# Performance work log

Measured on AMD Instinct MI355X. Metric: run time of the kernel, lower is better.

## Reference

```python
import jax, jax.numpy as jnp
import numpy as np

IN_F = 1024
OUT_F = 1024

def setup_inputs() -> dict:
    key = jax.random.key(0)
    ks = jax.random.split(key, 7)
    s = 1.0 / np.sqrt(IN_F)
    x = jax.random.normal(ks[0], (4, 2048, IN_F), dtype=jnp.float32)
    Wq = jax.random.uniform(ks[1], (OUT_F, IN_F), jnp.float32, -s, s)
    bq = jax.random.uniform(ks[2], (OUT_F,), jnp.float32, -s, s)
    Wk = jax.random.uniform(ks[3], (OUT_F, IN_F), jnp.float32, -s, s)
    bk = jax.random.uniform(ks[4], (OUT_F,), jnp.float32, -s, s)
    Wv = jax.random.uniform(ks[5], (OUT_F, IN_F), jnp.float32, -s, s)
    bv = jax.random.uniform(ks[6], (OUT_F,), jnp.float32, -s, s)
    return {"x": x, "Wq": Wq, "bq": bq, "Wk": Wk, "bk": bk, "Wv": Wv, "bv": bv}

def reference(x, Wq, bq, Wk, bk, Wv, bv):
    # Projector: ReLU(Linear(x))
    q = jax.nn.relu(jnp.einsum('bsd,od->bso', x, Wq) + bq)  # [B,S,O]
    k = jax.nn.relu(jnp.einsum('bsd,od->bso', x, Wk) + bk)
    v = jax.nn.relu(jnp.einsum('bsd,od->bso', x, Wv) + bv)
    logits = jnp.einsum('bio,bko->bik', q, k)  # unscaled QK^T, [B,S,S]
    scores = jax.nn.softmax(logits, axis=-1)
    out = jnp.einsum('bik,bko->bio', scores, v)
    return out
```

## Files before the change

kernel.cpp:

```cpp
#include <hip/hip_runtime.h>
#include <hip/hip_bf16.h>


#define SEQ 2048
#define DIM 1024
#define NB 4
#define MTOT (NB * SEQ)

typedef __attribute__((ext_vector_type(8))) short frag_ab;
typedef __attribute__((ext_vector_type(16))) float frag_c16;

__device__ __forceinline__ ushort f2bf(float f) {
    union { float f; unsigned u; } x; x.f = f;
    unsigned r = x.u + 0x7fffu + ((x.u >> 16) & 1u);
    return (ushort)(r >> 16);
}

typedef __attribute__((address_space(1))) const unsigned int guint;
typedef __attribute__((address_space(3))) unsigned int luint;

__device__ __forceinline__ void gld_lds16(const void* g, void* l) {
    __builtin_amdgcn_global_load_lds((guint*)g, (luint*)l, 16, 0, 0);
}

__device__ __forceinline__ void gemm_tiles(
    const ushort* __restrict__ A, size_t lda,
    const ushort* __restrict__ B, size_t ldb, int K,
    ushort* As, ushort* Bs, frag_c16 (&acc)[2][2])
{
    const int tid  = threadIdx.x;
    const int wave = tid >> 6;
    const int lane = tid & 63;
    const int l32  = lane & 31;
    const int half = lane >> 5;
    const int sr = wave * 16 + (lane >> 2);
    const int sc = lane & 3;
    const int wm = (wave & 1) * 64;
    const int wn = (wave >> 1) * 64;

    for (int k0 = 0; k0 < K; k0 += 32) {
        #pragma unroll
        for (int j = 0; j < 2; ++j) {
            int row = j * 64 + sr;
            int cg  = sc ^ ((row >> 1) & 3);
            ushort* la = As + (j * 64 + wave * 16) * 32;
            ushort* lb = Bs + (j * 64 + wave * 16) * 32;
            gld_lds16(A + (size_t)row * lda + k0 + cg * 8, la);
            gld_lds16(B + (size_t)row * ldb + k0 + cg * 8, lb);
        }
        __syncthreads();
        frag_ab af[2][2], bfr[2][2];
        #pragma unroll
        for (int mi = 0; mi < 2; ++mi) {
            int row = wm + mi * 32 + l32;
            int sw = (row >> 1) & 3;
            #pragma unroll
            for (int h = 0; h < 2; ++h) {
                int c = (h * 2 + half) ^ sw;
                af[mi][h] = *(const frag_ab*)&As[row * 32 + c * 8];
            }
        }
        #pragma unroll
        for (int ni = 0; ni < 2; ++ni) {
            int row = wn + ni * 32 + l32;
            int sw = (row >> 1) & 3;
            #pragma unroll
            for (int h = 0; h < 2; ++h) {
                int c = (h * 2 + half) ^ sw;
                bfr[ni][h] = *(const frag_ab*)&Bs[row * 32 + c * 8];
            }
        }
        #pragma unroll
        for (int h = 0; h < 2; ++h)
            #pragma unroll
            for (int mi = 0; mi < 2; ++mi)
                #pragma unroll
                for (int ni = 0; ni < 2; ++ni)
                    acc[mi][ni] = __builtin_amdgcn_mfma_f32_32x32x16_bf16(
                        af[mi][h], bfr[ni][h], acc[mi][ni], 0, 0, 0);
        __syncthreads();
    }
}


#define NX4 (MTOT * DIM / 4)
#define NW4 (DIM * DIM / 4)
__global__ __launch_bounds__(256) void cvt_kernel(
    const float* __restrict__ x,
    const float* __restrict__ Wq, const float* __restrict__ Wk,
    const float* __restrict__ Wv,
    ushort* __restrict__ xb, ushort* __restrict__ Wb)
{
    size_t i = (size_t)blockIdx.x * 256 + threadIdx.x;
    const float* src; ushort* dst; size_t idx;
    if (i < NX4) { src = x; dst = xb; idx = i; }
    else {
        size_t j = i - NX4;
        int w = (int)(j >> 18);
        idx = j & (NW4 - 1);
        src = w == 0 ? Wq : (w == 1 ? Wk : Wv);
        dst = Wb + (size_t)w * DIM * DIM;
    }
    float4 f = ((const float4*)src)[idx];
    ushort4 u; u.x = f2bf(f.x); u.y = f2bf(f.y); u.z = f2bf(f.z); u.w = f2bf(f.w);
    ((ushort4*)dst)[idx] = u;
}

__global__ __launch_bounds__(256) void qkv_kernel(
    const ushort* __restrict__ xb, const ushort* __restrict__ Wb,
    const float* __restrict__ bq, const float* __restrict__ bk,
    const float* __restrict__ bv,
    ushort* __restrict__ q, ushort* __restrict__ kk, ushort* __restrict__ vt)
{
    const float* bias;
    if (blockIdx.z == 0)      bias = bq;
    else if (blockIdx.z == 1) bias = bk;
    else                      bias = bv;
    const ushort* W = Wb + (size_t)blockIdx.z * DIM * DIM;

    __shared__ ushort As[128 * 32];
    __shared__ ushort Bs[128 * 32];

    const int tid  = threadIdx.x;
    const int wave = tid >> 6;
    const int lane = tid & 63;
    const int l32  = lane & 31;
    const int half = lane >> 5;
    const int m0 = blockIdx.x * 128;
    const int n0 = blockIdx.y * 128;
    const int wm = (wave & 1) * 64;
    const int wn = (wave >> 1) * 64;

    frag_c16 acc[2][2] = {};
    gemm_tiles(xb + (size_t)m0 * DIM, DIM, W + (size_t)n0 * DIM, DIM, DIM,
               As, Bs, acc);

    if (blockIdx.z == 2) {
        const int bz = m0 >> 11;
        const int sb = (m0 & (SEQ - 1)) + wm;
        #pragma unroll
        for (int ni = 0; ni < 2; ++ni) {
            int col = n0 + wn + ni * 32 + l32;
            float bb = bias[col];
            ushort* vrow = vt + ((size_t)(bz * DIM + col)) * SEQ;
            #pragma unroll
            for (int mi = 0; mi < 2; ++mi)
                #pragma unroll
                for (int g = 0; g < 4; ++g) {
                    int s0 = sb + mi * 32 + 8 * g + 4 * half;
                    ushort4 u;
                    #pragma unroll
                    for (int j = 0; j < 4; ++j) {
                        float val = acc[mi][ni][4 * g + j] + bb;
                        val = val > 0.0f ? val : 0.0f;
                        ((ushort*)&u)[j] = f2bf(val);
                    }
                    *(ushort4*)&vrow[s0] = u;
                }
        }
    } else {
        ushort* out = blockIdx.z == 0 ? q : kk;
        #pragma unroll
        for (int ni = 0; ni < 2; ++ni) {
            int col = n0 + wn + ni * 32 + l32;
            float bb = bias[col];
            #pragma unroll
            for (int mi = 0; mi < 2; ++mi)
                #pragma unroll
                for (int r = 0; r < 16; ++r) {
                    int row = m0 + wm + mi * 32 + (r & 3) + 8 * (r >> 2) + 4 * half;
                    float val = acc[mi][ni][r] + bb;
                    val = val > 0.0f ? val : 0.0f;
                    out[(size_t)row * DIM + col] = f2bf(val);
                }
        }
    }
}

__global__ __launch_bounds__(256) void qk_kernel(
    const ushort* __restrict__ q, const ushort* __restrict__ kk,
    float* __restrict__ logits)
{
    __shared__ ushort As[128 * 32];
    __shared__ ushort Bs[128 * 32];

    const int tid  = threadIdx.x;
    const int wave = tid >> 6;
    const int lane = tid & 63;
    const int l32  = lane & 31;
    const int half = lane >> 5;
    const int bz = blockIdx.z;
    const int m0 = blockIdx.x * 128;
    const int n0 = blockIdx.y * 128;
    const int wm = (wave & 1) * 64;
    const int wn = (wave >> 1) * 64;
    const size_t base = (size_t)bz * SEQ;

    frag_c16 acc[2][2] = {};
    gemm_tiles(q + (base + m0) * DIM, DIM, kk + (base + n0) * DIM, DIM, DIM,
               As, Bs, acc);

    #pragma unroll
    for (int mi = 0; mi < 2; ++mi)
        #pragma unroll
        for (int r = 0; r < 16; ++r) {
            int row = m0 + wm + mi * 32 + (r & 3) + 8 * (r >> 2) + 4 * half;
            #pragma unroll
            for (int ni = 0; ni < 2; ++ni) {
                int col = n0 + wn + ni * 32 + l32;
                logits[(base + row) * SEQ + col] = acc[mi][ni][r];
            }
        }
}

__global__ __launch_bounds__(256) void softmax_kernel(float* __restrict__ logits)
{
    const int row  = blockIdx.x * 4 + (threadIdx.x >> 6);
    const int lane = threadIdx.x & 63;
    float* p = logits + (size_t)row * SEQ;

    float4 x[8];
    #pragma unroll
    for (int i = 0; i < 8; ++i) x[i] = ((const float4*)p)[lane + 64 * i];

    float m = -3.4e38f;
    #pragma unroll
    for (int i = 0; i < 8; ++i)
        m = fmaxf(m, fmaxf(fmaxf(x[i].x, x[i].y), fmaxf(x[i].z, x[i].w)));
    #pragma unroll
    for (int off = 32; off; off >>= 1) m = fmaxf(m, __shfl_xor(m, off, 64));

    float s = 0.0f;
    #pragma unroll
    for (int i = 0; i < 8; ++i) {
        x[i].x = __expf(x[i].x - m); x[i].y = __expf(x[i].y - m);
        x[i].z = __expf(x[i].z - m); x[i].w = __expf(x[i].w - m);
        s += (x[i].x + x[i].y) + (x[i].z + x[i].w);
    }
    #pragma unroll
    for (int off = 32; off; off >>= 1) s += __shfl_xor(s, off, 64);
    float inv = 1.0f / s;

    ushort* o = (ushort*)p;
    #pragma unroll
    for (int i = 0; i < 8; ++i) {
        ushort4 u;
        u.x = f2bf(x[i].x * inv); u.y = f2bf(x[i].y * inv);
        u.z = f2bf(x[i].z * inv); u.w = f2bf(x[i].w * inv);
        ((ushort4*)o)[lane + 64 * i] = u;
    }
}

__global__ __launch_bounds__(256) void pv_kernel(
    const ushort* __restrict__ probs, const ushort* __restrict__ vt,
    float* __restrict__ out)
{
    __shared__ ushort As[128 * 32];
    __shared__ ushort Bs[128 * 32];

    const int tid  = threadIdx.x;
    const int wave = tid >> 6;
    const int lane = tid & 63;
    const int l32  = lane & 31;
    const int half = lane >> 5;
    const int bz = blockIdx.z;
    const int m0 = blockIdx.x * 128;
    const int n0 = blockIdx.y * 128;
    const int wm = (wave & 1) * 64;
    const int wn = (wave >> 1) * 64;

    frag_c16 acc[2][2] = {};
    gemm_tiles(probs + ((size_t)(bz * SEQ + m0)) * 4096, 4096,
               vt + ((size_t)(bz * DIM + n0)) * SEQ, SEQ, SEQ,
               As, Bs, acc);

    #pragma unroll
    for (int mi = 0; mi < 2; ++mi)
        #pragma unroll
        for (int r = 0; r < 16; ++r) {
            int row = m0 + wm + mi * 32 + (r & 3) + 8 * (r >> 2) + 4 * half;
            #pragma unroll
            for (int ni = 0; ni < 2; ++ni) {
                int col = n0 + wn + ni * 32 + l32;
                out[((size_t)(bz * SEQ + row)) * DIM + col] = acc[mi][ni][r];
            }
        }
}

extern "C" void kernel_launch(void* const* d_in, const int* in_sizes, int n_in,
                              void* d_out, int out_size, void* d_ws, size_t ws_size,
                              hipStream_t stream)
{
    const float* x  = (const float*)d_in[0];
    const float* Wq = (const float*)d_in[1];
    const float* bq = (const float*)d_in[2];
    const float* Wk = (const float*)d_in[3];
    const float* bk = (const float*)d_in[4];
    const float* Wv = (const float*)d_in[5];
    const float* bv = (const float*)d_in[6];
    float* out = (float*)d_out;

    char* ws = (char*)d_ws;
    ushort* q      = (ushort*)(ws);
    ushort* kk     = (ushort*)(ws + ((size_t)16 << 20));
    ushort* vt     = (ushort*)(ws + ((size_t)48 << 20));
    float*  logits = (float*) (ws + ((size_t)64 << 20));
    ushort* xb     = (ushort*)(ws + ((size_t)64 << 20));
    ushort* Wb     = (ushort*)(ws + ((size_t)80 << 20));

    cvt_kernel<<<dim3((NX4 + 3 * NW4) / 256), 256, 0, stream>>>(
        x, Wq, Wk, Wv, xb, Wb);

    qkv_kernel<<<dim3(MTOT / 128, DIM / 128, 3), 256, 0, stream>>>(
        xb, Wb, bq, bk, bv, q, kk, vt);
    qk_kernel<<<dim3(SEQ / 128, SEQ / 128, NB), 256, 0, stream>>>(q, kk, logits);
    softmax_kernel<<<NB * SEQ / 4, 256, 0, stream>>>(logits);
    pv_kernel<<<dim3(SEQ / 128, DIM / 128, NB), 256, 0, stream>>>(
        (const ushort*)logits, vt, out);
}
```

Measured before the change: 280.4 us.

## Double-buffer LDS tiles in shared GEMM loop with async prefetch

The shared GEMM tile loop now uses two LDS buffers. It issues the global-to-LDS loads for the next K tile before computing on the current one, waits with an explicit vmcnt and uses raw s_barrier instead of two __syncthreads per iteration. This is meant to hide global load latency behind MFMA work in the projection, QK and PV kernels. It doubles LDS use per block, which may lower occupancy, and the final iteration issues a redundant reload of the last tile.

Result: slower. 292.5 us (+4.3%).

```diff
diff --git a/kernel.cpp b/kernel.cpp
--- a/kernel.cpp
+++ b/kernel.cpp
@@ -22,6 +22,15 @@
 __device__ __forceinline__ void gld_lds16(const void* g, void* l) {
     __builtin_amdgcn_global_load_lds((guint*)g, (luint*)l, 16, 0, 0);
 }
+
+__device__ __forceinline__ void bar() {
+    asm volatile("" ::: "memory");
+    __builtin_amdgcn_s_barrier();
+    asm volatile("" ::: "memory");
+}
+#define VMCNT(n) asm volatile("s_waitcnt vmcnt(" #n ")" ::: "memory")
+
+#define TB (128 * 32)
 
 __device__ __forceinline__ void gemm_tiles(
     const ushort* __restrict__ A, size_t lda,
@@ -37,18 +46,31 @@
     const int sc = lane & 3;
     const int wm = (wave & 1) * 64;
     const int wn = (wave >> 1) * 64;
-
-    for (int k0 = 0; k0 < K; k0 += 32) {
-        #pragma unroll
-        for (int j = 0; j < 2; ++j) {
-            int row = j * 64 + sr;
-            int cg  = sc ^ ((row >> 1) & 3);
-            ushort* la = As + (j * 64 + wave * 16) * 32;
-            ushort* lb = Bs + (j * 64 + wave * 16) * 32;
-            gld_lds16(A + (size_t)row * lda + k0 + cg * 8, la);
-            gld_lds16(B + (size_t)row * ldb + k0 + cg * 8, lb);
-        }
-        __syncthreads();
+    const int nkt = K >> 5;
+
+    #define STAGE_TILE(kt, b) do {                                          \
+        int k0_ = (kt) << 5;                                                \
+        _Pragma("unroll")                                                   \
+        for (int j = 0; j < 2; ++j) {                                       \
+            int row = j * 64 + sr;                                          \
+            int cg  = sc ^ ((row >> 1) & 3);                                \
+            ushort* la = As + (b) * TB + (j * 64 + wave * 16) * 32;         \
+            ushort* lb = Bs + (b) * TB + (j * 64 + wave * 16) * 32;         \
+            gld_lds16(A + (size_t)row * lda + k0_ + cg * 8, la);            \
+            gld_lds16(B + (size_t)row * ldb + k0_ + cg * 8, lb);            \
+        }                                                                   \
+    } while (0)
+
+    STAGE_TILE(0, 0);
+    for (int t = 0; t < nkt; ++t) {
+        const int c = t & 1;
+        int tn = t + 1 < nkt ? t + 1 : nkt - 1;
+        STAGE_TILE(tn, c ^ 1);
+        VMCNT(4);
+        bar();
+
+        const ushort* Ac = As + c * TB;
+        const ushort* Bc = Bs + c * TB;
         frag_ab af[2][2], bfr[2][2];
         #pragma unroll
         for (int mi = 0; mi < 2; ++mi) {
@@ -56,8 +78,8 @@
             int sw = (row >> 1) & 3;
             #pragma unroll
             for (int h = 0; h < 2; ++h) {
-                int c = (h * 2 + half) ^ sw;
-                af[mi][h] = *(const frag_ab*)&As[row * 32 + c * 8];
+                int cc = (h * 2 + half) ^ sw;
+                af[mi][h] = *(const frag_ab*)&Ac[row * 32 + cc * 8];
             }
         }
         #pragma unroll
@@ -66,10 +88,14 @@
             int sw = (row >> 1) & 3;
             #pragma unroll
             for (int h = 0; h < 2; ++h) {
-                int c = (h * 2 + half) ^ sw;
-                bfr[ni][h] = *(const frag_ab*)&Bs[row * 32 + c * 8];
+                int cc = (h * 2 + half) ^ sw;
+                bfr[ni][h] = *(const frag_ab*)&Bc[row * 32 + cc * 8];
             }
         }
+        asm volatile("s_waitcnt lgkmcnt(0)" ::: "memory");
+        __builtin_amdgcn_sched_barrier(0);
+        bar();
+
         #pragma unroll
         for (int h = 0; h < 2; ++h)
             #pragma unroll
@@ -78,8 +104,9 @@
                 for (int ni = 0; ni < 2; ++ni)
                     acc[mi][ni] = __builtin_amdgcn_mfma_f32_32x32x16_bf16(
                         af[mi][h], bfr[ni][h], acc[mi][ni], 0, 0, 0);
-        __syncthreads();
-    }
+    }
+    VMCNT(0);
+    #undef STAGE_TILE
 }
 
 
@@ -118,8 +145,8 @@
     else                      bias = bv;
     const ushort* W = Wb + (size_t)blockIdx.z * DIM * DIM;
 
-    __shared__ ushort As[128 * 32];
-    __shared__ ushort Bs[128 * 32];
+    __shared__ ushort As[2 * TB];
+    __shared__ ushort Bs[2 * TB];
 
     const int tid  = threadIdx.x;
     const int wave = tid >> 6;
@@ -181,8 +208,8 @@
     const ushort* __restrict__ q, const ushort* __restrict__ kk,
     float* __restrict__ logits)
 {
-    __shared__ ushort As[128 * 32];
-    __shared__ ushort Bs[128 * 32];
+    __shared__ ushort As[2 * TB];
+    __shared__ ushort Bs[2 * TB];
 
     const int tid  = threadIdx.x;
     const int wave = tid >> 6;
@@ -255,8 +282,8 @@
     const ushort* __restrict__ probs, const ushort* __restrict__ vt,
     float* __restrict__ out)
 {
-    __shared__ ushort As[128 * 32];
-    __shared__ ushort Bs[128 * 32];
+    __shared__ ushort As[2 * TB];
+    __shared__ ushort Bs[2 * TB];
 
     const int tid  = threadIdx.x;
     const int wave = tid >> 6;
```
